# Optimization experiments

Hardware: AMD Instinct MI355X
Metric: run time of the kernel (lower is better)

## Reference

```python
import jax, jax.numpy as jnp
import numpy as np

WS = 7        # window_size
SHIFT = 3     # shift_size
HEADS = 6
DIM = 192
HIDDEN = DIM * 6  # mlp_ratio=6
EPS = 1e-5


def _rel_pos_index(ws):
    # static relative-position index, (ws*ws, ws*ws) int
    coords = np.stack(np.meshgrid(np.arange(ws), np.arange(ws), indexing='ij')).reshape(2, -1)
    rel = coords[:, :, None] - coords[:, None, :]            # (2, N, N)
    rel = rel.transpose(1, 2, 0)                             # (N, N, 2)
    rel[:, :, 0] += ws - 1
    rel[:, :, 1] += ws - 1
    rel[:, :, 0] *= 2 * ws - 1
    return rel.sum(-1)


def _layernorm(t, g, b):
    m = t.mean(-1, keepdims=True)
    v = jnp.mean((t - m) ** 2, axis=-1, keepdims=True)
    return (t - m) * jax.lax.rsqrt(v + EPS) * g + b


def setup_inputs() -> dict:
    key = jax.random.key(0)
    ks = jax.random.split(key, 8)
    B, H, W = 16, 56, 56
    x = jax.random.normal(ks[0], (B, H * W, DIM), dtype=jnp.float32)
    p = lambda k, s: (jax.random.normal(k, s, dtype=jnp.float32) * 0.02)
    return {
        'x': x, 'H': H, 'W': W,
        'ln1_g': jnp.ones((DIM,), jnp.float32), 'ln1_b': jnp.zeros((DIM,), jnp.float32),
        'qkv_w': p(ks[1], (3 * DIM, DIM)), 'qkv_b': jnp.zeros((3 * DIM,), jnp.float32),
        'rpb': p(ks[2], ((2 * WS - 1) ** 2, HEADS)),
        'proj_w': p(ks[3], (DIM, DIM)), 'proj_b': jnp.zeros((DIM,), jnp.float32),
        'ln2_g': jnp.ones((DIM,), jnp.float32), 'ln2_b': jnp.zeros((DIM,), jnp.float32),
        'fc1_w': p(ks[4], (HIDDEN, DIM)), 'fc1_b': jnp.zeros((HIDDEN,), jnp.float32),
        'fc2_w': p(ks[5], (DIM, HIDDEN)), 'fc2_b': jnp.zeros((DIM,), jnp.float32),
    }


def reference(x, H, W, ln1_g, ln1_b, qkv_w, qkv_b, rpb, proj_w, proj_b,
              ln2_g, ln2_b, fc1_w, fc1_b, fc2_w, fc2_b):
    B, L, C = x.shape
    hd = C // HEADS
    shortcut = x
    h = _layernorm(x, ln1_g, ln1_b).reshape(B, H, W, C)
    pad_r = (WS - W % WS) % WS
    pad_b = (WS - H % WS) % WS
    h = jnp.pad(h, ((0, 0), (0, pad_b), (0, pad_r), (0, 0)))
    Hp, Wp = H + pad_b, W + pad_r
    if SHIFT > 0:
        h = jnp.roll(h, (-SHIFT, -SHIFT), axis=(1, 2))
    # window partition -> (nW*B, WS*WS, C)
    h = h.reshape(B, Hp // WS, WS, Wp // WS, WS, C).transpose(0, 1, 3, 2, 4, 5)
    h = h.reshape(-1, WS * WS, C)
    nB, N, _ = h.shape
    qkv = (h @ qkv_w.T + qkv_b).reshape(nB, N, 3, HEADS, hd).transpose(2, 0, 3, 1, 4)
    q, k, v = qkv[0], qkv[1], qkv[2]       # (nB, heads, N, hd)
    scale = hd ** -0.5
    attn = jnp.einsum('bhnd,bhmd->bhnm', q * scale, k)
    idx = _rel_pos_index(WS)
    bias = rpb[idx.reshape(-1)].reshape(N, N, HEADS).transpose(2, 0, 1)  # (heads, N, N)
    attn = jax.nn.softmax(attn + bias[None], axis=-1)
    out = jnp.einsum('bhnm,bhmd->bhnd', attn, v).transpose(0, 2, 1, 3).reshape(nB, N, C)
    out = out @ proj_w.T + proj_b
    # window reverse -> (B, Hp, Wp, C)
    out = out.reshape(B, Hp // WS, Wp // WS, WS, WS, C).transpose(0, 1, 3, 2, 4, 5)
    out = out.reshape(B, Hp, Wp, C)
    if SHIFT > 0:
        out = jnp.roll(out, (SHIFT, SHIFT), axis=(1, 2))
    out = out[:, :H, :W, :].reshape(B, H * W, C)
    x = shortcut + out
    h2 = _layernorm(x, ln2_g, ln2_b)
    h2 = jax.nn.gelu(h2 @ fc1_w.T + fc1_b, approximate=False)
    return x + (h2 @ fc2_w.T + fc2_b)
```

## Files before the change

### kernel.cpp

```cpp
#include <hip/hip_runtime.h>

typedef unsigned short u16;
typedef __bf16 bf16x8 __attribute__((ext_vector_type(8)));
typedef __bf16 bf16x2_t __attribute__((ext_vector_type(2)));
typedef float f32x4 __attribute__((ext_vector_type(4)));

#define AS1 __attribute__((address_space(1)))
#define AS3 __attribute__((address_space(3)))

__device__ __forceinline__ void gld16(const void* g, void* l) {
  __builtin_amdgcn_global_load_lds((const AS1 void*)g, (AS3 void*)l, 16, 0, 0);
}

__device__ __forceinline__ u16 f2bf(float f) {
  union { float f; unsigned int u; } v; v.f = f;
  unsigned int u = v.u;
  u += 0x7fffu + ((u >> 16) & 1u);
  return (u16)(u >> 16);
}
__device__ __forceinline__ float bf2f(u16 h) {
  union { unsigned int u; float f; } v; v.u = ((unsigned int)h) << 16; return v.f;
}
__device__ __forceinline__ unsigned int pk2(float a, float b) {
#if __has_builtin(__builtin_amdgcn_cvt_pk_bf16_f32)
  union { bf16x2_t v; unsigned int u; } c;
  c.v = __builtin_amdgcn_cvt_pk_bf16_f32(a, b);
  return c.u;
#else
  return (unsigned int)f2bf(a) | ((unsigned int)f2bf(b) << 16);
#endif
}
__device__ __forceinline__ float gelu_f(float v) {
  float u = v * (1.5957691216f + 0.0713548163f * v * v);
  return v * __builtin_amdgcn_rcpf(1.0f + __expf(-u));
}

__global__ __launch_bounds__(256) void cast_weights(
    const float* __restrict__ w0, const float* __restrict__ w1,
    const float* __restrict__ w2, const float* __restrict__ w3,
    u16* __restrict__ o0, u16* __restrict__ o1,
    u16* __restrict__ o2, u16* __restrict__ o3) {
  int i = blockIdx.x * 256 + threadIdx.x;
  if (i < 110592) o0[i] = f2bf(w0[i]);
  if (i < 36864) {
    int n = i / 192, kp = i - n * 192;
    int h = kp >> 5, dp = kp & 31;
    int d = (dp & 1) ? ((dp >> 1) + 16) : (dp >> 1);
    o1[i] = f2bf(w1[n * 192 + h * 32 + d]);
  }
  if (i < 221184) o2[i] = f2bf(w2[i]);
  if (i < 221184) o3[i] = f2bf(w3[i]);
}

__global__ __launch_bounds__(256) void build_btab(
    const float* __restrict__ rpb, float* __restrict__ btab) {
  int id = blockIdx.x * 256 + threadIdx.x;
  int head = id >> 12;
  int m = (id >> 6) & 63;
  int r = id & 63;
  float v;
  if (m >= 49) v = -1e30f;
  else if (r >= 49) v = 0.0f;
  else {
    int mi = m / 7, mj = m - mi * 7;
    int ri = r / 7, rj = r - ri * 7;
    v = rpb[((ri - mi + 6) * 13 + (rj - mj + 6)) * 6 + head];
  }
  btab[id] = v;
}

__global__ __launch_bounds__(256) void ln_kernel(
    const float* __restrict__ x, const float* __restrict__ g,
    const float* __restrict__ b, u16* __restrict__ out) {
  int row = blockIdx.x * 4 + (threadIdx.x >> 6);
  int lane = threadIdx.x & 63;
  const float* xr = x + (long)row * 192;
  float e0 = xr[lane], e1 = xr[lane + 64], e2 = xr[lane + 128];
  float s = e0 + e1 + e2;
  #pragma unroll
  for (int o = 1; o < 64; o <<= 1) s += __shfl_xor(s, o);
  float mean = s * (1.0f / 192.0f);
  float d0 = e0 - mean, d1 = e1 - mean, d2 = e2 - mean;
  float q = d0 * d0 + d1 * d1 + d2 * d2;
  #pragma unroll
  for (int o = 1; o < 64; o <<= 1) q += __shfl_xor(q, o);
  float rstd = rsqrtf(q * (1.0f / 192.0f) + 1e-5f);
  u16* orow = out + (long)row * 192;
  orow[lane]       = f2bf(d0 * rstd * g[lane]       + b[lane]);
  orow[lane + 64]  = f2bf(d1 * rstd * g[lane + 64]  + b[lane + 64]);
  orow[lane + 128] = f2bf(d2 * rstd * g[lane + 128] + b[lane + 128]);
}

template<int MODE>
__global__ __launch_bounds__(256, 3) void wsgemm_kernel(
    const u16* __restrict__ A, const u16* __restrict__ W,
    const float* __restrict__ bias, const float* __restrict__ resid,
    void* __restrict__ out, int N) {
  __shared__ u16 wlds[36 * 512];
  const int tid = threadIdx.x;
  const int wave = tid >> 6, lane = tid & 63;
  const int quad = lane >> 4, l15 = lane & 15;
  const int bn = blockIdx.y * 96;
  const long bm = (long)blockIdx.x * 128 + wave * 32;

  bf16x8 af[2][6];
  #pragma unroll
  for (int mt = 0; mt < 2; mt++)
    #pragma unroll
    for (int kc = 0; kc < 6; kc++)
      af[mt][kc] = *(const bf16x8*)&A[(bm + mt * 16 + l15) * 192 + kc * 32 + quad * 8];

  #pragma unroll
  for (int i = 0; i < 9; i++) {
    int t = wave + i * 4;
    int kc = t / 6, nt = t - kc * 6;
    gld16(W + (long)(bn + nt * 16 + l15) * 192 + kc * 32 + quad * 8,
          &wlds[t * 512]);
  }

  float bi[6];
  #pragma unroll
  for (int nt = 0; nt < 6; nt++) bi[nt] = bias[bn + nt * 16 + l15];

  __syncthreads();

  f32x4 acc[2][6] = {};
  #pragma unroll
  for (int kc = 0; kc < 6; kc++) {
    #pragma unroll
    for (int nt = 0; nt < 6; nt++) {
      bf16x8 wf = *(const bf16x8*)&wlds[(kc * 6 + nt) * 512 + lane * 8];
      acc[0][nt] = __builtin_amdgcn_mfma_f32_16x16x32_bf16(af[0][kc], wf, acc[0][nt], 0, 0, 0);
      acc[1][nt] = __builtin_amdgcn_mfma_f32_16x16x32_bf16(af[1][kc], wf, acc[1][nt], 0, 0, 0);
    }
  }

  #pragma unroll
  for (int mt = 0; mt < 2; mt++) {
    #pragma unroll
    for (int nt = 0; nt < 6; nt++) {
      const long col = bn + nt * 16 + l15;
      #pragma unroll
      for (int j = 0; j < 4; j++) {
        const long row = bm + mt * 16 + quad * 4 + j;
        const long idx = row * (long)N + col;
        float v = acc[mt][nt][j] + bi[nt];
        if (MODE == 2) {
          ((float*)out)[idx] = v + resid[idx];
        } else {
          if (MODE == 1) v = gelu_f(v);
          ((u16*)out)[idx] = f2bf(v);
        }
      }
    }
  }
}

__global__ __launch_bounds__(256, 3) void wsgemm2_kernel(
    const u16* __restrict__ A, const u16* __restrict__ W,
    const float* __restrict__ bias, const float* __restrict__ resid,
    float* __restrict__ out, int N) {
  __shared__ u16 wlds[36 * 512];
  const int tid = threadIdx.x;
  const int wave = tid >> 6, lane = tid & 63;
  const int quad = lane >> 4, l15 = lane & 15;
  const int bn = blockIdx.y * 96;
  const long bm = (long)blockIdx.x * 128 + wave * 32;

  const u16* pa0 = A + (bm + l15) * 1152 + quad * 8;
  const u16* pa1 = pa0 + 16 * 1152;
  const u16* wp[9];
  int wd[9];
  #pragma unroll
  for (int i = 0; i < 9; i++) {
    int t = wave + i * 4;
    int kc = t / 6, nt = t - kc * 6;
    wp[i] = W + (long)(bn + nt * 16 + l15) * 1152 + kc * 32 + quad * 8;
    wd[i] = t * 512;
  }

  f32x4 acc[2][6] = {};
  #pragma unroll
  for (int c = 0; c < 6; c++) {
    if (c) __syncthreads();
    bf16x8 af0[6], af1[6];
    #pragma unroll
    for (int kc = 0; kc < 6; kc++) {
      af0[kc] = *(const bf16x8*)(pa0 + kc * 32);
      af1[kc] = *(const bf16x8*)(pa1 + kc * 32);
    }
    #pragma unroll
    for (int i = 0; i < 9; i++) gld16(wp[i], &wlds[wd[i]]);
    __syncthreads();
    #pragma unroll
    for (int kc = 0; kc < 6; kc++) {
      #pragma unroll
      for (int nt = 0; nt < 6; nt++) {
        bf16x8 wf = *(const bf16x8*)&wlds[(kc * 6 + nt) * 512 + lane * 8];
        acc[0][nt] = __builtin_amdgcn_mfma_f32_16x16x32_bf16(af0[kc], wf, acc[0][nt], 0, 0, 0);
        acc[1][nt] = __builtin_amdgcn_mfma_f32_16x16x32_bf16(af1[kc], wf, acc[1][nt], 0, 0, 0);
      }
    }
    pa0 += 192; pa1 += 192;
    #pragma unroll
    for (int i = 0; i < 9; i++) wp[i] += 192;
  }

  float bi[6];
  #pragma unroll
  for (int nt = 0; nt < 6; nt++) bi[nt] = bias[bn + nt * 16 + l15];
  #pragma unroll
  for (int mt = 0; mt < 2; mt++) {
    #pragma unroll
    for (int nt = 0; nt < 6; nt++) {
      const long col = bn + nt * 16 + l15;
      #pragma unroll
      for (int j = 0; j < 4; j++) {
        const long row = bm + mt * 16 + quad * 4 + j;
        const long idx = row * (long)N + col;
        out[idx] = acc[mt][nt][j] + bi[nt] + resid[idx];
      }
    }
  }
}

__global__ __launch_bounds__(256) void attn_kernel(
    const u16* __restrict__ qkv, const float* __restrict__ btab,
    u16* __restrict__ attn) {
  __shared__ u16 lds[4 * 7040];
  __shared__ float sbias[64 * 65];
  int tid = threadIdx.x;
  int wave = tid >> 6, lane = tid & 63;
  int quad = lane >> 4, l15 = lane & 15;
  int head = blockIdx.x % 6;
  int grp = blockIdx.x / 6;
  int win = grp * 4 + wave;
  int b = win >> 6, wy = (win >> 3) & 7, wx = win & 7;
  u16* lp = lds + wave * 7040;
  u16* lvt = lp + 4608;
  float* rsum = (float*)(lp + 6912);

  {
    const float* bsrc = btab + head * 4096;
    #pragma unroll
    for (int i = 0; i < 4; i++) {
      int idx4 = tid + i * 256;
      float4 v = *(const float4*)(bsrc + idx4 * 4);
      float* dst = &sbias[(idx4 >> 4) * 65 + (idx4 & 15) * 4];
      dst[0] = v.x; dst[1] = v.y; dst[2] = v.z; dst[3] = v.w;
    }
  }

  bf16x8 qb[4], ka[4];
  #pragma unroll
  for (int t = 0; t < 4; t++) {
    int n = t * 16 + l15;
    uint4 qv = {0, 0, 0, 0}, kv = {0, 0, 0, 0}, vv = {0, 0, 0, 0};
    if (n < 49) {
      int i = n / 7, j = n - i * 7;
      int y = wy * 7 + i + 3;  if (y >= 56) y -= 56;
      int xx = wx * 7 + j + 3; if (xx >= 56) xx -= 56;
      long base = ((long)(b * 3136 + y * 56 + xx)) * 576 + head * 32 + quad * 8;
      qv = *(const uint4*)(qkv + base);
      kv = *(const uint4*)(qkv + base + 192);
      vv = *(const uint4*)(qkv + base + 384);
    }
    qb[t] = *(const bf16x8*)&qv;
    ka[t] = *(const bf16x8*)&kv;
    const u16* vp = (const u16*)&vv;
    #pragma unroll
    for (int d = 0; d < 8; d++) lvt[(quad * 8 + d) * 72 + n] = vp[d];
  }

  f32x4 s[4][4];
  const f32x4 fz = {0.0f, 0.0f, 0.0f, 0.0f};
  #pragma unroll
  for (int tm = 0; tm < 4; tm++)
    #pragma unroll
    for (int tr = 0; tr < 4; tr++)
      s[tm][tr] = __builtin_amdgcn_mfma_f32_16x16x32_bf16(ka[tm], qb[tr], fz, 0, 0, 0);

  __syncthreads();

  const float scale = 0.17677669529663687f;
  float mx[4] = {-1e30f, -1e30f, -1e30f, -1e30f};
  #pragma unroll
  for (int tm = 0; tm < 4; tm++) {
    int m0 = tm * 16 + quad * 4;
    #pragma unroll
    for (int tr = 0; tr < 4; tr++) {
      int r = tr * 16 + l15;
      #pragma unroll
      for (int j = 0; j < 4; j++) {
        float v = s[tm][tr][j] * scale + sbias[(m0 + j) * 65 + r];
        s[tm][tr][j] = v;
        mx[tr] = fmaxf(mx[tr], v);
      }
    }
  }
  #pragma unroll
  for (int tr = 0; tr < 4; tr++) {
    mx[tr] = fmaxf(mx[tr], __shfl_xor(mx[tr], 16));
    mx[tr] = fmaxf(mx[tr], __shfl_xor(mx[tr], 32));
  }
  float sm[4] = {0.f, 0.f, 0.f, 0.f};
  #pragma unroll
  for (int tm = 0; tm < 4; tm++) {
    #pragma unroll
    for (int tr = 0; tr < 4; tr++) {
      int r = tr * 16 + l15;
      float e0 = __expf(s[tm][tr][0] - mx[tr]);
      float e1 = __expf(s[tm][tr][1] - mx[tr]);
      float e2 = __expf(s[tm][tr][2] - mx[tr]);
      float e3 = __expf(s[tm][tr][3] - mx[tr]);
      sm[tr] += (e0 + e1) + (e2 + e3);
      uint2 pk;
      pk.x = pk2(e0, e1);
      pk.y = pk2(e2, e3);
      *(uint2*)&lp[r * 72 + tm * 16 + quad * 4] = pk;
    }
  }
  #pragma unroll
  for (int tr = 0; tr < 4; tr++) {
    sm[tr] += __shfl_xor(sm[tr], 16);
    sm[tr] += __shfl_xor(sm[tr], 32);
  }
  if (quad == 0) {
    #pragma unroll
    for (int tr = 0; tr < 4; tr++) rsum[tr * 16 + l15] = __builtin_amdgcn_rcpf(sm[tr]);
  }

  f32x4 o[4][2] = {};
  #pragma unroll
  for (int ks = 0; ks < 2; ks++) {
    bf16x8 vb0 = *(const bf16x8*)&lvt[(l15) * 72 + ks * 32 + quad * 8];
    bf16x8 vb1 = *(const bf16x8*)&lvt[(16 + l15) * 72 + ks * 32 + quad * 8];
    #pragma unroll
    for (int rt = 0; rt < 4; rt++) {
      bf16x8 pf = *(const bf16x8*)&lp[(rt * 16 + l15) * 72 + ks * 32 + quad * 8];
      o[rt][0] = __builtin_amdgcn_mfma_f32_16x16x32_bf16(pf, vb0, o[rt][0], 0, 0, 0);
      o[rt][1] = __builtin_amdgcn_mfma_f32_16x16x32_bf16(pf, vb1, o[rt][1], 0, 0, 0);
    }
  }
  #pragma unroll
  for (int rt = 0; rt < 4; rt++) {
    #pragma unroll
    for (int j = 0; j < 4; j++) {
      int r = rt * 16 + quad * 4 + j;
      if (r < 49) {
        float inv = rsum[r];
        int i = r / 7, jj = r - i * 7;
        int y = wy * 7 + i + 3;   if (y >= 56) y -= 56;
        int xx = wx * 7 + jj + 3; if (xx >= 56) xx -= 56;
        long base = ((long)(b * 3136 + y * 56 + xx)) * 192 + head * 32 + 2 * l15;
        *(unsigned int*)&attn[base] = pk2(o[rt][0][j] * inv, o[rt][1][j] * inv);
      }
    }
  }
}

extern "C" void kernel_launch(void* const* d_in, const int* in_sizes, int n_in,
                              void* d_out, int out_size, void* d_ws, size_t ws_size,
                              hipStream_t stream) {
  (void)in_sizes; (void)n_in; (void)out_size; (void)ws_size;
  const float* x      = (const float*)d_in[0];
  const float* ln1_g  = (const float*)d_in[3];
  const float* ln1_b  = (const float*)d_in[4];
  const float* qkv_w  = (const float*)d_in[5];
  const float* qkv_b  = (const float*)d_in[6];
  const float* rpb    = (const float*)d_in[7];
  const float* proj_w = (const float*)d_in[8];
  const float* proj_b = (const float*)d_in[9];
  const float* ln2_g  = (const float*)d_in[10];
  const float* ln2_b  = (const float*)d_in[11];
  const float* fc1_w  = (const float*)d_in[12];
  const float* fc1_b  = (const float*)d_in[13];
  const float* fc2_w  = (const float*)d_in[14];
  const float* fc2_b  = (const float*)d_in[15];

  char* ws = (char*)d_ws;
  float* x2   = (float*)(ws + 0);
  u16* hA     = (u16*)(ws + 38535168);
  float* btab = (float*)(ws + 38535168);
  u16* qkv    = (u16*)(ws + 57802752);
  u16* attn   = (u16*)(ws + 115605504);
  u16* hid    = (u16*)(ws + 57802752);
  u16* wbuf   = (u16*)(ws + 173408256);
  u16* qkv_wb  = wbuf;
  u16* proj_wb = wbuf + 110592;
  u16* fc1_wb  = wbuf + 147456;
  u16* fc2_wb  = wbuf + 368640;

  cast_weights<<<dim3(864), 256, 0, stream>>>(qkv_w, proj_w, fc1_w, fc2_w,
                                              qkv_wb, proj_wb, fc1_wb, fc2_wb);
  ln_kernel<<<dim3(12544), 256, 0, stream>>>(x, ln1_g, ln1_b, hA);
  wsgemm_kernel<0><<<dim3(392, 6), 256, 0, stream>>>(hA, qkv_wb, qkv_b, nullptr,
                                                     qkv, 576);
  build_btab<<<dim3(96), 256, 0, stream>>>(rpb, btab);
  attn_kernel<<<dim3(1536), 256, 0, stream>>>(qkv, btab, attn);
  wsgemm_kernel<2><<<dim3(392, 2), 256, 0, stream>>>(attn, proj_wb, proj_b, x,
                                                     x2, 192);
  ln_kernel<<<dim3(12544), 256, 0, stream>>>(x2, ln2_g, ln2_b, hA);
  wsgemm_kernel<1><<<dim3(392, 12), 256, 0, stream>>>(hA, fc1_wb, fc1_b, nullptr,
                                                      hid, 1152);
  wsgemm2_kernel<<<dim3(392, 2), 256, 0, stream>>>(hid, fc2_wb, fc2_b, x2,
                                                   (float*)d_out, 192);
}
```

Before: 359.4 us.

## Double-buffer fc2 GEMM weight staging and templatize GEMM N-tile count

The fc2 GEMM kernel now uses two LDS weight buffers and two A-fragment register sets. It prefetches the next K-chunk's weights and activations while running MFMAs on the current chunk, which removes one barrier per chunk. The general GEMM kernel gains an NT template parameter for the N-tile width, but every launch still uses NT=6, so that part changes nothing yet. The double buffering doubles LDS use and register pressure, and lowers the launch-bounds occupancy hint to 2 blocks per CU.

```diff
diff --git a/kernel.cpp b/kernel.cpp
--- a/kernel.cpp
+++ b/kernel.cpp
@@ -91,16 +91,17 @@
   orow[lane + 128] = f2bf(d2 * rstd * g[lane + 128] + b[lane + 128]);
 }
 
-template<int MODE>
-__global__ __launch_bounds__(256, 3) void wsgemm_kernel(
+template<int MODE, int NT>
+__global__ __launch_bounds__(256, (NT == 12) ? 2 : 3) void wsgemm_kernel(
     const u16* __restrict__ A, const u16* __restrict__ W,
     const float* __restrict__ bias, const float* __restrict__ resid,
     void* __restrict__ out, int N) {
-  __shared__ u16 wlds[36 * 512];
+  constexpr int TILES = 6 * NT;
+  __shared__ u16 wlds[TILES * 512];
   const int tid = threadIdx.x;
   const int wave = tid >> 6, lane = tid & 63;
   const int quad = lane >> 4, l15 = lane & 15;
-  const int bn = blockIdx.y * 96;
+  const int bn = blockIdx.y * (16 * NT);
   const long bm = (long)blockIdx.x * 128 + wave * 32;
 
   bf16x8 af[2][6];
@@ -111,25 +112,25 @@
       af[mt][kc] = *(const bf16x8*)&A[(bm + mt * 16 + l15) * 192 + kc * 32 + quad * 8];
 
   #pragma unroll
-  for (int i = 0; i < 9; i++) {
+  for (int i = 0; i < TILES / 4; i++) {
     int t = wave + i * 4;
-    int kc = t / 6, nt = t - kc * 6;
+    int kc = t / NT, nt = t - kc * NT;
     gld16(W + (long)(bn + nt * 16 + l15) * 192 + kc * 32 + quad * 8,
           &wlds[t * 512]);
   }
 
-  float bi[6];
-  #pragma unroll
-  for (int nt = 0; nt < 6; nt++) bi[nt] = bias[bn + nt * 16 + l15];
-
-  __syncthreads();
-
-  f32x4 acc[2][6] = {};
+  float bi[NT];
+  #pragma unroll
+  for (int nt = 0; nt < NT; nt++) bi[nt] = bias[bn + nt * 16 + l15];
+
+  __syncthreads();
+
+  f32x4 acc[2][NT] = {};
   #pragma unroll
   for (int kc = 0; kc < 6; kc++) {
     #pragma unroll
-    for (int nt = 0; nt < 6; nt++) {
-      bf16x8 wf = *(const bf16x8*)&wlds[(kc * 6 + nt) * 512 + lane * 8];
+    for (int nt = 0; nt < NT; nt++) {
+      bf16x8 wf = *(const bf16x8*)&wlds[(kc * NT + nt) * 512 + lane * 8];
       acc[0][nt] = __builtin_amdgcn_mfma_f32_16x16x32_bf16(af[0][kc], wf, acc[0][nt], 0, 0, 0);
       acc[1][nt] = __builtin_amdgcn_mfma_f32_16x16x32_bf16(af[1][kc], wf, acc[1][nt], 0, 0, 0);
     }
@@ -138,7 +139,7 @@
   #pragma unroll
   for (int mt = 0; mt < 2; mt++) {
     #pragma unroll
-    for (int nt = 0; nt < 6; nt++) {
+    for (int nt = 0; nt < NT; nt++) {
       const long col = bn + nt * 16 + l15;
       #pragma unroll
       for (int j = 0; j < 4; j++) {
@@ -156,11 +157,11 @@
   }
 }
 
-__global__ __launch_bounds__(256, 3) void wsgemm2_kernel(
+__global__ __launch_bounds__(256, 2) void wsgemm2db_kernel(
     const u16* __restrict__ A, const u16* __restrict__ W,
     const float* __restrict__ bias, const float* __restrict__ resid,
     float* __restrict__ out, int N) {
-  __shared__ u16 wlds[36 * 512];
+  __shared__ u16 wlds[2][36 * 512];
   const int tid = threadIdx.x;
   const int wave = tid >> 6, lane = tid & 63;
   const int quad = lane >> 4, l15 = lane & 15;
@@ -179,32 +180,53 @@
     wd[i] = t * 512;
   }
 
+  auto stageW = [&](int c, int b) {
+    #pragma unroll
+    for (int i = 0; i < 9; i++) gld16(wp[i] + c * 192, &wlds[b][wd[i]]);
+  };
+
+  bf16x8 afA[2][6], afB[2][6];
+  auto ldA = [&](bf16x8 (&af)[2][6], int c) {
+    #pragma unroll
+    for (int kc = 0; kc < 6; kc++) {
+      af[0][kc] = *(const bf16x8*)(pa0 + c * 192 + kc * 32);
+      af[1][kc] = *(const bf16x8*)(pa1 + c * 192 + kc * 32);
+    }
+  };
+
   f32x4 acc[2][6] = {};
-  #pragma unroll
-  for (int c = 0; c < 6; c++) {
-    if (c) __syncthreads();
-    bf16x8 af0[6], af1[6];
-    #pragma unroll
-    for (int kc = 0; kc < 6; kc++) {
-      af0[kc] = *(const bf16x8*)(pa0 + kc * 32);
-      af1[kc] = *(const bf16x8*)(pa1 + kc * 32);
-    }
-    #pragma unroll
-    for (int i = 0; i < 9; i++) gld16(wp[i], &wlds[wd[i]]);
-    __syncthreads();
+  auto compute = [&](int b, bf16x8 (&af)[2][6]) {
     #pragma unroll
     for (int kc = 0; kc < 6; kc++) {
       #pragma unroll
       for (int nt = 0; nt < 6; nt++) {
-        bf16x8 wf = *(const bf16x8*)&wlds[(kc * 6 + nt) * 512 + lane * 8];
-        acc[0][nt] = __builtin_amdgcn_mfma_f32_16x16x32_bf16(af0[kc], wf, acc[0][nt], 0, 0, 0);
-        acc[1][nt] = __builtin_amdgcn_mfma_f32_16x16x32_bf16(af1[kc], wf, acc[1][nt], 0, 0, 0);
+        bf16x8 wf = *(const bf16x8*)&wlds[b][(kc * 6 + nt) * 512 + lane * 8];
+        acc[0][nt] = __builtin_amdgcn_mfma_f32_16x16x32_bf16(af[0][kc], wf, acc[0][nt], 0, 0, 0);
+        acc[1][nt] = __builtin_amdgcn_mfma_f32_16x16x32_bf16(af[1][kc], wf, acc[1][nt], 0, 0, 0);
       }
     }
-    pa0 += 192; pa1 += 192;
-    #pragma unroll
-    for (int i = 0; i < 9; i++) wp[i] += 192;
-  }
+  };
+
+  ldA(afA, 0);
+  stageW(0, 0);
+  __syncthreads();
+
+  ldA(afB, 1); stageW(1, 1);
+  compute(0, afA);
+  __syncthreads();
+  ldA(afA, 2); stageW(2, 0);
+  compute(1, afB);
+  __syncthreads();
+  ldA(afB, 3); stageW(3, 1);
+  compute(0, afA);
+  __syncthreads();
+  ldA(afA, 4); stageW(4, 0);
+  compute(1, afB);
+  __syncthreads();
+  ldA(afB, 5); stageW(5, 1);
+  compute(0, afA);
+  __syncthreads();
+  compute(1, afB);
 
   float bi[6];
   #pragma unroll
@@ -394,15 +416,15 @@
   cast_weights<<<dim3(864), 256, 0, stream>>>(qkv_w, proj_w, fc1_w, fc2_w,
                                               qkv_wb, proj_wb, fc1_wb, fc2_wb);
   ln_kernel<<<dim3(12544), 256, 0, stream>>>(x, ln1_g, ln1_b, hA);
-  wsgemm_kernel<0><<<dim3(392, 6), 256, 0, stream>>>(hA, qkv_wb, qkv_b, nullptr,
-                                                     qkv, 576);
+  wsgemm_kernel<0, 6><<<dim3(392, 6), 256, 0, stream>>>(hA, qkv_wb, qkv_b, nullptr,
+                                                        qkv, 576);
   build_btab<<<dim3(96), 256, 0, stream>>>(rpb, btab);
   attn_kernel<<<dim3(1536), 256, 0, stream>>>(qkv, btab, attn);
-  wsgemm_kernel<2><<<dim3(392, 2), 256, 0, stream>>>(attn, proj_wb, proj_b, x,
-                                                     x2, 192);
+  wsgemm_kernel<2, 6><<<dim3(392, 2), 256, 0, stream>>>(attn, proj_wb, proj_b, x,
+                                                        x2, 192);
   ln_kernel<<<dim3(12544), 256, 0, stream>>>(x2, ln2_g, ln2_b, hA);
-  wsgemm_kernel<1><<<dim3(392, 12), 256, 0, stream>>>(hA, fc1_wb, fc1_b, nullptr,
-                                                      hid, 1152);
-  wsgemm2_kernel<<<dim3(392, 2), 256, 0, stream>>>(hid, fc2_wb, fc2_b, x2,
-                                                   (float*)d_out, 192);
-}
+  wsgemm_kernel<1, 6><<<dim3(392, 12), 256, 0, stream>>>(hA, fc1_wb, fc1_b, nullptr,
+                                                         hid, 1152);
+  wsgemm2db_kernel<<<dim3(392, 2), 256, 0, stream>>>(hid, fc2_wb, fc2_b, x2,
+                                                     (float*)d_out, 192);
+}
```

Result: no change. 361.1 us (+0.5%).
